# Kernel optimization log

Hardware: AMD Instinct MI355X
Metric: run time of the kernel (lower is better)

The kernel has to match this reference:

```python
import jax, jax.numpy as jnp
import numpy as np

B, N_L, N_T, C_IN, HID, NG, ATOMS, N_EDGES = 8, 128, 512, 128, 128, 10, 24, 4096
BN_EPS = 1e-5


def setup_inputs() -> dict:
    key = jax.random.key(0)
    ks = jax.random.split(key, 20)
    f32 = jnp.float32
    s = 0.05  # weight scale
    return {
        "h_l_x": jax.random.normal(ks[0], (B, N_L, C_IN), f32),
        "h_t_x": jax.random.normal(ks[1], (B, N_T, C_IN), f32),
        "l_mask": jnp.ones((B, N_L), dtype=bool),
        "t_mask": jnp.ones((B, N_T), dtype=bool),
        "h_l_pos": jax.random.normal(ks[2], (B, N_L, 3), f32),
        "h_t_pos": jax.random.normal(ks[3], (B, N_T * ATOMS, 3), f32),
        "x_l_flat": jax.random.normal(ks[4], (B * N_L, C_IN), f32),
        "edge_index": jax.random.randint(ks[5], (2, N_EDGES), 0, B * N_L),
        "W1": jax.random.normal(ks[6], (2 * C_IN, HID), f32) * s,
        "b1": jnp.zeros((HID,), f32),
        "bn_gamma": jnp.ones((HID,), f32),
        "bn_beta": jnp.zeros((HID,), f32),
        "bn_mean": jnp.zeros((HID,), f32),
        "bn_var": jnp.ones((HID,), f32),
        "W_pi": jax.random.normal(ks[7], (HID, NG), f32) * s,
        "b_pi": jnp.zeros((NG,), f32),
        "W_sigma": jax.random.normal(ks[8], (HID, NG), f32) * s,
        "b_sigma": jnp.zeros((NG,), f32),
        "W_mu": jax.random.normal(ks[9], (HID, NG), f32) * s,
        "b_mu": jnp.zeros((NG,), f32),
        "W_nuc": jax.random.normal(ks[10], (C_IN, 12), f32) * s,
        "b_nuc": jnp.zeros((12,), f32),
        "W_bond": jax.random.normal(ks[11], (2 * C_IN, 4), f32) * s,
        "b_bond": jnp.zeros((4,), f32),
    }


def reference(h_l_x, h_t_x, l_mask, t_mask, h_l_pos, h_t_pos, x_l_flat, edge_index,
              W1, b1, bn_gamma, bn_beta, bn_mean, bn_var,
              W_pi, b_pi, W_sigma, b_sigma, W_mu, b_mu,
              W_nuc, b_nuc, W_bond, b_bond):
    Bsz, Nl, Cd = h_l_x.shape
    Nt = h_t_x.shape[1]
    # dense pairwise concat: [B, N_l, N_t, 2C] (masks are all-True, so the
    # boolean selection C[C_mask] of the original is a static flatten)
    pair = jnp.concatenate([
        jnp.broadcast_to(h_l_x[:, :, None, :], (Bsz, Nl, Nt, Cd)),
        jnp.broadcast_to(h_t_x[:, None, :, :], (Bsz, Nl, Nt, Cd)),
    ], axis=-1).reshape(-1, 2 * Cd)
    # MLP: Linear -> BatchNorm1d (eval, running stats) -> ELU -> Dropout(eval=id)
    h = pair @ W1 + b1
    h = (h - bn_mean) * jax.lax.rsqrt(bn_var + BN_EPS) * bn_gamma + bn_beta
    h = jax.nn.elu(h)
    # MDN heads
    pi = jax.nn.softmax(h @ W_pi + b_pi, axis=-1)
    sigma = jax.nn.elu(h @ W_sigma + b_sigma) + 1.1
    mu = jax.nn.elu(h @ W_mu + b_mu) + 1.0
    # auxiliary heads on flat ligand node features
    nuc_types = x_l_flat @ W_nuc + b_nuc
    bond_feat = jnp.concatenate([x_l_flat[edge_index[0]], x_l_flat[edge_index[1]]], axis=1)
    bond_types = bond_feat @ W_bond + b_bond
    # pairwise distances with windowed min over 24 atoms per target residue
    d2 = (-2.0 * jnp.einsum('bld,btd->blt', h_l_pos, h_t_pos)
          + jnp.sum(h_t_pos ** 2, axis=-1)[:, None, :]
          + jnp.sum(h_l_pos ** 2, axis=-1)[:, :, None])
    d = jnp.nan_to_num(jnp.sqrt(d2), nan=10000.0)  # nan from sqrt(<0)
    dist = d.reshape(Bsz, Nl, Nt, ATOMS).min(axis=-1)  # [B, N_l, N_t]
    dist = jax.lax.stop_gradient(dist.reshape(-1)[:, None])  # detached, [M,1]
    C_batch = jnp.broadcast_to(jnp.arange(Bsz)[:, None, None], (Bsz, Nl, Nt)).reshape(-1)
    return (pi, sigma, mu, dist, nuc_types, bond_types, C_batch)
```

## Files before the change

### kernel.cpp

```cpp
#include <hip/hip_runtime.h>

#define B_      8
#define N_L     128
#define N_T     512
#define C_IN    128
#define HID     128
#define NG      10
#define ATOMS   24
#define N_EDGES 4096

#define OFF_PI  0
#define OFF_SG  5242880
#define OFF_MU  10485760
#define OFF_DI  15728640
#define OFF_NU  16252928
#define OFF_BO  16265216
#define OFF_CB  16281600

#define WS_U    0
#define WS_V    131072
#define WS_B    659456
#define WS_WT   659488

typedef unsigned short u16;
typedef unsigned int   u32;
typedef short s16x8 __attribute__((ext_vector_type(8)));
typedef float f32x4 __attribute__((ext_vector_type(4)));
typedef float f32x16 __attribute__((ext_vector_type(16)));
typedef u32   u32x4 __attribute__((ext_vector_type(4)));

__device__ __forceinline__ float bfu2f(u16 s) {
  u32 u = ((u32)s) << 16;
  return __builtin_bit_cast(float, u);
}
__device__ __forceinline__ u16 f2bf(float f) {
  u32 u = __builtin_bit_cast(u32, f);
  u32 r = (u + 0x7fffu + ((u >> 16) & 1u)) >> 16;
  return (u16)r;
}
__device__ __forceinline__ u32 pack2(float a, float b) {
  return (u32)f2bf(a) | ((u32)f2bf(b) << 16);
}
__device__ __forceinline__ u32 pkhi(float hi, float lo) {
  return __builtin_amdgcn_perm(__builtin_bit_cast(u32, hi),
                               __builtin_bit_cast(u32, lo), 0x07060302u);
}
__device__ __forceinline__ float eluf(float x) {
  return x > 0.f ? x : __expf(x) - 1.f;
}
__device__ __forceinline__ s16x8 ld8(const u16* p) {
  return __builtin_bit_cast(s16x8, *(const u32x4*)p);
}

template<bool F32>
__device__ __forceinline__ float ldf(const void* p, size_t i) {
  if constexpr (F32) return ((const float*)p)[i];
  else               return bfu2f(((const u16*)p)[i]);
}
template<bool F32>
__device__ __forceinline__ u16 wraw(const void* p, size_t i) {
  if constexpr (F32) return f2bf(((const float*)p)[i]);
  else               return ((const u16*)p)[i];
}
__device__ __forceinline__ bool is_f32(const u32* probe) {
  return (probe[0] & 0xFFFFu) == 0u;
}

template<bool F32>
__device__ __forceinline__ void prep_rows(
    int blk, int tid,
    const void* hlx, const void* htx, const void* W1, const void* b1,
    const void* gam, const void* bet, const void* mean_, const void* var_,
    float* __restrict__ ws, float (*xs)[C_IN]) {
  int k = tid & 127, g = tid >> 7;
  bool isU = (blk < 128);
  const void* x = isU ? hlx : htx;
  int row0 = isU ? blk * 8 : (blk - 128) * 8;
  size_t woff = isU ? 0 : (size_t)C_IN * HID;
  #pragma unroll
  for (int i = 0; i < 4; ++i) {
    int e = tid + i * 256;
    int rr = e >> 7, cc = e & 127;
    xs[rr][cc] = ldf<F32>(x, (size_t)(row0 + rr) * C_IN + cc);
  }
  __syncthreads();
  float a0 = 0.f, a1 = 0.f, a2 = 0.f, a3 = 0.f;
  const float* xr0 = xs[g * 4 + 0];
  const float* xr1 = xs[g * 4 + 1];
  const float* xr2 = xs[g * 4 + 2];
  const float* xr3 = xs[g * 4 + 3];
  #pragma unroll 8
  for (int c = 0; c < C_IN; ++c) {
    float w = ldf<F32>(W1, woff + (size_t)c * HID + k);
    a0 += xr0[c] * w;
    a1 += xr1[c] * w;
    a2 += xr2[c] * w;
    a3 += xr3[c] * w;
  }
  float A = ldf<F32>(gam, k) * rsqrtf(ldf<F32>(var_, k) + 1e-5f);
  float add = 0.f;
  if (isU) add = ldf<F32>(b1, k) * A + (ldf<F32>(bet, k) - ldf<F32>(mean_, k) * A);
  float* dst = ws + (isU ? WS_U : WS_V) + (size_t)row0 * HID;
  dst[(g * 4 + 0) * HID + k] = a0 * A + add;
  dst[(g * 4 + 1) * HID + k] = a1 * A + add;
  dst[(g * 4 + 2) * HID + k] = a2 * A + add;
  dst[(g * 4 + 3) * HID + k] = a3 * A + add;
}

template<bool F32>
__device__ __forceinline__ void prep_consts(
    int tid, const void* Wpi, const void* bpi, const void* Wsg, const void* bsg,
    const void* Wmu, const void* bmu, float* __restrict__ ws) {
  if (tid >= 128) return;
  int k = tid;
  u16* wt = (u16*)(ws + WS_WT);
  for (int j = 0; j < 32; ++j) {
    u16 val = 0;
    if (j < 10)      val = wraw<F32>(Wpi, (size_t)k * NG + j);
    else if (j < 20) val = wraw<F32>(Wsg, (size_t)k * NG + j - 10);
    else if (j < 30) val = wraw<F32>(Wmu, (size_t)k * NG + j - 20);
    wt[(size_t)j * HID + k] = val;
  }
  if (k < 32) {
    float bb = 0.f;
    if (k < 10)      bb = ldf<F32>(bpi, k);
    else if (k < 20) bb = ldf<F32>(bsg, k - 10);
    else if (k < 30) bb = ldf<F32>(bmu, k - 20);
    ws[WS_B + k] = bb;
  }
}

template<bool F32>
__device__ __forceinline__ void dist_impl(int blk2,
                                          const void* __restrict__ lpos,
                                          const void* __restrict__ tpos,
                                          void* __restrict__ out) {
  int lc   = blk2 & 63;
  int half = (blk2 >> 6) & 1;
  int b    = blk2 >> 7;
  int t = half * 256 + threadIdx.x;

  size_t tbase = ((size_t)b * (N_T * ATOMS) + (size_t)t * ATOMS) * 3;
  float ax[ATOMS], ay[ATOMS], az[ATOMS], an[ATOMS];
  if constexpr (F32) {
    float c[72];
    const float4* tp4 = (const float4*)((const float*)tpos + tbase);
    #pragma unroll
    for (int i = 0; i < 18; ++i) {
      float4 qv = tp4[i];
      c[4*i+0] = qv.x; c[4*i+1] = qv.y; c[4*i+2] = qv.z; c[4*i+3] = qv.w;
    }
    #pragma unroll
    for (int a = 0; a < ATOMS; ++a) {
      ax[a] = c[3*a]; ay[a] = c[3*a+1]; az[a] = c[3*a+2];
      an[a] = ax[a]*ax[a] + ay[a]*ay[a] + az[a]*az[a];
    }
  } else {
    u32 raw[36];
    const uint4* tp4 = (const uint4*)((const u16*)tpos + tbase);
    #pragma unroll
    for (int i = 0; i < 9; ++i) {
      uint4 qv = tp4[i];
      raw[4*i+0] = qv.x; raw[4*i+1] = qv.y; raw[4*i+2] = qv.z; raw[4*i+3] = qv.w;
    }
    #pragma unroll
    for (int a = 0; a < ATOMS; ++a) {
      int e = 3 * a;
      u32 w0 = raw[e >> 1];
      ax[a] = bfu2f((e & 1) ? (u16)(w0 >> 16) : (u16)w0);
      u32 w1 = raw[(e + 1) >> 1];
      ay[a] = bfu2f(((e + 1) & 1) ? (u16)(w1 >> 16) : (u16)w1);
      u32 w2 = raw[(e + 2) >> 1];
      az[a] = bfu2f(((e + 2) & 1) ? (u16)(w2 >> 16) : (u16)w2);
      an[a] = ax[a]*ax[a] + ay[a]*ay[a] + az[a]*az[a];
    }
  }
  #pragma unroll
  for (int il = 0; il < 2; ++il) {
    int l = lc * 2 + il;
    size_t lbase = ((size_t)b * N_L + l) * 3;
    float lx = ldf<F32>(lpos, lbase), ly = ldf<F32>(lpos, lbase+1), lz = ldf<F32>(lpos, lbase+2);
    float ln = lx*lx + ly*ly + lz*lz;
    float m = 1e30f;
    #pragma unroll
    for (int a = 0; a < ATOMS; ++a) {
      float dot = ax[a]*lx + ay[a]*ly + az[a]*lz;
      float d2 = ln + an[a] - 2.f * dot;
      d2 = (d2 >= 0.f) ? d2 : 1e30f;
      m = fminf(m, d2);
    }
    float d = (m < 1e29f) ? sqrtf(m) : 10000.0f;
    long p = ((long)(b * N_L + l)) * N_T + t;
    if constexpr (F32) {
      ((float*)out)[OFF_DI + p] = d;
      ((float*)out)[OFF_CB + p] = (float)b;
    } else {
      ((u16*)out)[OFF_DI + p] = f2bf(d);
      ((u16*)out)[OFF_CB + p] = f2bf((float)b);
    }
  }
}

__global__ __launch_bounds__(256) void prep_fused(
    const void* hlx, const void* htx, const void* W1, const void* b1,
    const void* gam, const void* bet, const void* mean_, const void* var_,
    const void* Wpi, const void* bpi, const void* Wsg, const void* bsg,
    const void* Wmu, const void* bmu, float* ws,
    const void* lpos, const void* tpos, void* out, const u32* probe) {
  __shared__ float xs[8][C_IN];
  int blk = blockIdx.x;
  int tid = threadIdx.x;
  bool f = is_f32(probe);
  if (blk < 640) {
    if (f) prep_rows<true >(blk, tid, hlx, htx, W1, b1, gam, bet, mean_, var_, ws, xs);
    else   prep_rows<false>(blk, tid, hlx, htx, W1, b1, gam, bet, mean_, var_, ws, xs);
  } else if (blk == 640) {
    if (f) prep_consts<true >(tid, Wpi, bpi, Wsg, bsg, Wmu, bmu, ws);
    else   prep_consts<false>(tid, Wpi, bpi, Wsg, bsg, Wmu, bmu, ws);
  } else {
    int blk2 = blk - 641;
    if (f) dist_impl<true >(blk2, lpos, tpos, out);
    else   dist_impl<false>(blk2, lpos, tpos, out);
  }
}

template<bool F32>
__device__ __forceinline__ void nuc_wave(int r, int lane, const void* __restrict__ xl,
    const void* __restrict__ Wnu, const void* __restrict__ bnu, void* __restrict__ out) {
  float x0 = ldf<F32>(xl, (size_t)r * C_IN + lane);
  float x1 = ldf<F32>(xl, (size_t)r * C_IN + 64 + lane);
  #pragma unroll
  for (int j = 0; j < 12; ++j) {
    float a = x0 * ldf<F32>(Wnu, (size_t)lane * 12 + j)
            + x1 * ldf<F32>(Wnu, (size_t)(64 + lane) * 12 + j);
    #pragma unroll
    for (int m = 32; m >= 1; m >>= 1) a += __shfl_xor(a, m);
    if (lane == 0) {
      float v = a + ldf<F32>(bnu, j);
      if constexpr (F32) ((float*)out)[OFF_NU + (size_t)r * 12 + j] = v;
      else               ((u16*)out)[OFF_NU + (size_t)r * 12 + j] = f2bf(v);
    }
  }
}

template<bool F32>
__device__ __forceinline__ void bond_wave(int e, int lane, const void* __restrict__ xl,
    const int* __restrict__ eidx, const void* __restrict__ Wbo,
    const void* __restrict__ bbo, void* __restrict__ out) {
  int e0 = eidx[e], e1 = eidx[N_EDGES + e];
  float x0 = ldf<F32>(xl, (size_t)e0 * C_IN + lane);
  float x1 = ldf<F32>(xl, (size_t)e0 * C_IN + 64 + lane);
  float y0 = ldf<F32>(xl, (size_t)e1 * C_IN + lane);
  float y1 = ldf<F32>(xl, (size_t)e1 * C_IN + 64 + lane);
  #pragma unroll
  for (int j = 0; j < 4; ++j) {
    float a = x0 * ldf<F32>(Wbo, (size_t)lane * 4 + j)
            + x1 * ldf<F32>(Wbo, (size_t)(64 + lane) * 4 + j)
            + y0 * ldf<F32>(Wbo, (size_t)(128 + lane) * 4 + j)
            + y1 * ldf<F32>(Wbo, (size_t)(192 + lane) * 4 + j);
    #pragma unroll
    for (int m = 32; m >= 1; m >>= 1) a += __shfl_xor(a, m);
    if (lane == 0) {
      float v = a + ldf<F32>(bbo, j);
      if constexpr (F32) ((float*)out)[OFF_BO + (size_t)e * 4 + j] = v;
      else               ((u16*)out)[OFF_BO + (size_t)e * 4 + j] = f2bf(v);
    }
  }
}

__global__ __launch_bounds__(256, 4) void main_fused(
    const float* __restrict__ ws, void* __restrict__ out, const u32* probe,
    const void* __restrict__ xl, const int* __restrict__ eidx,
    const void* __restrict__ Wnu, const void* __restrict__ bnu,
    const void* __restrict__ Wbo, const void* __restrict__ bbo) {
  __shared__ __align__(16) float stage[3840];
  __shared__ float u_lds[C_IN];
  int blk = blockIdx.x;
  int tid = threadIdx.x;
  int lane = tid & 63, wave = tid >> 6;
  bool f32o = is_f32(probe);

  if (blk >= 1024) {
    if (blk < 1024 + 256) {
      int r = (blk - 1024) * 4 + wave;
      if (f32o) nuc_wave<true >(r, lane, xl, Wnu, bnu, out);
      else      nuc_wave<false>(r, lane, xl, Wnu, bnu, out);
    } else {
      int e = (blk - 1280) * 4 + wave;
      if (f32o) bond_wave<true >(e, lane, xl, eidx, Wbo, bbo, out);
      else      bond_wave<false>(e, lane, xl, eidx, Wbo, bbo, out);
    }
    return;
  }

  int bl = blk;
  int b  = bl >> 7;
  int j  = lane & 31;
  int hi = lane >> 5;

  if (tid < C_IN) u_lds[tid] = ws[WS_U + (size_t)bl * HID + tid];
  __syncthreads();

  const u16* wt = (const u16*)(ws + WS_WT);
  s16x8 wf[8];
  #pragma unroll
  for (int ks = 0; ks < 8; ++ks)
    wf[ks] = ld8(wt + (size_t)j * HID + ks * 16 + hi * 8);

  float binit[16];
  #pragma unroll
  for (int r = 0; r < 16; ++r)
    binit[r] = ws[WS_B + ((r & 3) + 8 * (r >> 2) + 4 * hi)];

  const float* vbase = ws + WS_V + (size_t)b * N_T * HID;

  #pragma unroll 1
  for (int it = 0; it < 4; ++it) {
    int t = it * 128 + wave * 32 + j;
    const float* vp = vbase + (size_t)t * HID;

    f32x16 acc;
    #pragma unroll
    for (int r = 0; r < 16; ++r) acc[r] = binit[r];

    #pragma unroll
    for (int ks = 0; ks < 8; ++ks) {
      int ko = ks * 16 + hi * 8;
      f32x4 va = *(const f32x4*)(vp + ko);
      f32x4 vb = *(const f32x4*)(vp + ko + 4);
      f32x4 ua = *(const f32x4*)(u_lds + ko);
      f32x4 ub = *(const f32x4*)(u_lds + ko + 4);
      float h0 = eluf(va[0] + ua[0]);
      float h1 = eluf(va[1] + ua[1]);
      float h2 = eluf(va[2] + ua[2]);
      float h3 = eluf(va[3] + ua[3]);
      float h4 = eluf(vb[0] + ub[0]);
      float h5 = eluf(vb[1] + ub[1]);
      float h6 = eluf(vb[2] + ub[2]);
      float h7 = eluf(vb[3] + ub[3]);
      u32x4 hw = { pkhi(h1,h0), pkhi(h3,h2), pkhi(h5,h4), pkhi(h7,h6) };
      s16x8 hf = __builtin_bit_cast(s16x8, hw);
      acc = __builtin_amdgcn_mfma_f32_32x32x16_bf16(wf[ks], hf, acc, 0, 0, 0);
    }

    float pm = fmaxf(fmaxf(acc[0], acc[1]), fmaxf(acc[2], acc[3]));
    if (hi == 0) pm = fmaxf(pm, fmaxf(acc[4], acc[5]));
    pm = fmaxf(pm, __shfl_xor(pm, 32));
    float e0 = __expf(acc[0] - pm), e1 = __expf(acc[1] - pm);
    float e2 = __expf(acc[2] - pm), e3 = __expf(acc[3] - pm);
    float e4 = 0.f, e5 = 0.f;
    float es = e0 + e1 + e2 + e3;
    if (hi == 0) {
      e4 = __expf(acc[4] - pm); e5 = __expf(acc[5] - pm);
      es += e4 + e5;
    }
    es += __shfl_xor(es, 32);
    float inv = 1.f / es;

    int tl = wave * 32 + j;
    float* r0 = stage +        tl * 10;
    float* r1 = stage + 1280 + tl * 10;
    float* r2 = stage + 2560 + tl * 10;
    if (hi == 0) {
      r0[0] = e0*inv; r0[1] = e1*inv; r0[2] = e2*inv; r0[3] = e3*inv;
      r0[8] = e4*inv; r0[9] = e5*inv;
      r1[0] = eluf(acc[6])+1.1f;  r1[1] = eluf(acc[7])+1.1f;
      r1[6] = eluf(acc[8])+1.1f;  r1[7] = eluf(acc[9])+1.1f;
      r1[8] = eluf(acc[10])+1.1f; r1[9] = eluf(acc[11])+1.1f;
      r2[4] = eluf(acc[12])+1.0f; r2[5] = eluf(acc[13])+1.0f;
      r2[6] = eluf(acc[14])+1.0f; r2[7] = eluf(acc[15])+1.0f;
    } else {
      r0[4] = e0*inv; r0[5] = e1*inv; r0[6] = e2*inv; r0[7] = e3*inv;
      r1[2] = eluf(acc[4])+1.1f;  r1[3] = eluf(acc[5])+1.1f;
      r1[4] = eluf(acc[6])+1.1f;  r1[5] = eluf(acc[7])+1.1f;
      r2[0] = eluf(acc[8])+1.0f;  r2[1] = eluf(acc[9])+1.0f;
      r2[2] = eluf(acc[10])+1.0f; r2[3] = eluf(acc[11])+1.0f;
      r2[8] = eluf(acc[12])+1.0f; r2[9] = eluf(acc[13])+1.0f;
    }
    __syncthreads();

    size_t rowbase = ((size_t)bl * N_T + (size_t)it * 128) * NG;
    if (f32o) {
      float* o = (float*)out;
      #pragma unroll
      for (int g0 = 0; g0 < 4; ++g0) {
        int g = g0 * 256 + tid;
        if (g < 960) {
          int region = g / 320;
          int off = (g - region * 320) * 4;
          f32x4 v = *(const f32x4*)(stage + region * 1280 + off);
          size_t ob = (region == 0 ? (size_t)OFF_PI
                      : region == 1 ? (size_t)OFF_SG : (size_t)OFF_MU)
                      + rowbase + off;
          *(f32x4*)(o + ob) = v;
        }
      }
    } else {
      u16* o = (u16*)out;
      #pragma unroll
      for (int g0 = 0; g0 < 2; ++g0) {
        int g = g0 * 256 + tid;
        if (g < 480) {
          int region = g / 160;
          int off = (g - region * 160) * 8;
          const float* s = stage + region * 1280 + off;
          u32x4 v = { pack2(s[0],s[1]), pack2(s[2],s[3]),
                      pack2(s[4],s[5]), pack2(s[6],s[7]) };
          size_t ob = (region == 0 ? (size_t)OFF_PI
                      : region == 1 ? (size_t)OFF_SG : (size_t)OFF_MU)
                      + rowbase + off;
          *(u32x4*)(o + ob) = v;
        }
      }
    }
    __syncthreads();
  }
}

extern "C" void kernel_launch(void* const* d_in, const int* in_sizes, int n_in,
                              void* d_out, int out_size, void* d_ws, size_t ws_size,
                              hipStream_t stream) {
  int s = (n_in >= 24) ? 2 : 0;
  const void* hlx  = d_in[0];
  const void* htx  = d_in[1];
  const void* lpos = d_in[2 + s];
  const void* tpos = d_in[3 + s];
  const void* xl   = d_in[4 + s];
  const int*  eidx = (const int*)d_in[5 + s];
  const void* W1   = d_in[6 + s];
  const void* b1   = d_in[7 + s];
  const void* gam  = d_in[8 + s];
  const void* bet  = d_in[9 + s];
  const void* mean_= d_in[10 + s];
  const void* var_ = d_in[11 + s];
  const void* Wpi  = d_in[12 + s];
  const void* bpi  = d_in[13 + s];
  const void* Wsg  = d_in[14 + s];
  const void* bsg  = d_in[15 + s];
  const void* Wmu  = d_in[16 + s];
  const void* bmu  = d_in[17 + s];
  const void* Wnu  = d_in[18 + s];
  const void* bnu  = d_in[19 + s];
  const void* Wbo  = d_in[20 + s];
  const void* bbo  = d_in[21 + s];
  const u32* probe = (const u32*)var_;
  float* ws = (float*)d_ws;

  prep_fused<<<1665, 256, 0, stream>>>(hlx, htx, W1, b1, gam, bet, mean_, var_,
                                       Wpi, bpi, Wsg, bsg, Wmu, bmu, ws,
                                       lpos, tpos, d_out, probe);
  main_fused<<<2304, 256, 0, stream>>>(ws, d_out, probe,
                                       xl, eidx, Wnu, bnu, Wbo, bbo);
}
```

Before: 175.7 us.

## Move distance blocks into main kernel and use per-wave output staging

```diff
diff --git a/kernel.cpp b/kernel.cpp
--- a/kernel.cpp
+++ b/kernel.cpp
@@ -130,83 +130,11 @@
   }
 }
 
-template<bool F32>
-__device__ __forceinline__ void dist_impl(int blk2,
-                                          const void* __restrict__ lpos,
-                                          const void* __restrict__ tpos,
-                                          void* __restrict__ out) {
-  int lc   = blk2 & 63;
-  int half = (blk2 >> 6) & 1;
-  int b    = blk2 >> 7;
-  int t = half * 256 + threadIdx.x;
-
-  size_t tbase = ((size_t)b * (N_T * ATOMS) + (size_t)t * ATOMS) * 3;
-  float ax[ATOMS], ay[ATOMS], az[ATOMS], an[ATOMS];
-  if constexpr (F32) {
-    float c[72];
-    const float4* tp4 = (const float4*)((const float*)tpos + tbase);
-    #pragma unroll
-    for (int i = 0; i < 18; ++i) {
-      float4 qv = tp4[i];
-      c[4*i+0] = qv.x; c[4*i+1] = qv.y; c[4*i+2] = qv.z; c[4*i+3] = qv.w;
-    }
-    #pragma unroll
-    for (int a = 0; a < ATOMS; ++a) {
-      ax[a] = c[3*a]; ay[a] = c[3*a+1]; az[a] = c[3*a+2];
-      an[a] = ax[a]*ax[a] + ay[a]*ay[a] + az[a]*az[a];
-    }
-  } else {
-    u32 raw[36];
-    const uint4* tp4 = (const uint4*)((const u16*)tpos + tbase);
-    #pragma unroll
-    for (int i = 0; i < 9; ++i) {
-      uint4 qv = tp4[i];
-      raw[4*i+0] = qv.x; raw[4*i+1] = qv.y; raw[4*i+2] = qv.z; raw[4*i+3] = qv.w;
-    }
-    #pragma unroll
-    for (int a = 0; a < ATOMS; ++a) {
-      int e = 3 * a;
-      u32 w0 = raw[e >> 1];
-      ax[a] = bfu2f((e & 1) ? (u16)(w0 >> 16) : (u16)w0);
-      u32 w1 = raw[(e + 1) >> 1];
-      ay[a] = bfu2f(((e + 1) & 1) ? (u16)(w1 >> 16) : (u16)w1);
-      u32 w2 = raw[(e + 2) >> 1];
-      az[a] = bfu2f(((e + 2) & 1) ? (u16)(w2 >> 16) : (u16)w2);
-      an[a] = ax[a]*ax[a] + ay[a]*ay[a] + az[a]*az[a];
-    }
-  }
-  #pragma unroll
-  for (int il = 0; il < 2; ++il) {
-    int l = lc * 2 + il;
-    size_t lbase = ((size_t)b * N_L + l) * 3;
-    float lx = ldf<F32>(lpos, lbase), ly = ldf<F32>(lpos, lbase+1), lz = ldf<F32>(lpos, lbase+2);
-    float ln = lx*lx + ly*ly + lz*lz;
-    float m = 1e30f;
-    #pragma unroll
-    for (int a = 0; a < ATOMS; ++a) {
-      float dot = ax[a]*lx + ay[a]*ly + az[a]*lz;
-      float d2 = ln + an[a] - 2.f * dot;
-      d2 = (d2 >= 0.f) ? d2 : 1e30f;
-      m = fminf(m, d2);
-    }
-    float d = (m < 1e29f) ? sqrtf(m) : 10000.0f;
-    long p = ((long)(b * N_L + l)) * N_T + t;
-    if constexpr (F32) {
-      ((float*)out)[OFF_DI + p] = d;
-      ((float*)out)[OFF_CB + p] = (float)b;
-    } else {
-      ((u16*)out)[OFF_DI + p] = f2bf(d);
-      ((u16*)out)[OFF_CB + p] = f2bf((float)b);
-    }
-  }
-}
-
 __global__ __launch_bounds__(256) void prep_fused(
     const void* hlx, const void* htx, const void* W1, const void* b1,
     const void* gam, const void* bet, const void* mean_, const void* var_,
     const void* Wpi, const void* bpi, const void* Wsg, const void* bsg,
-    const void* Wmu, const void* bmu, float* ws,
-    const void* lpos, const void* tpos, void* out, const u32* probe) {
+    const void* Wmu, const void* bmu, float* ws, const u32* probe) {
   __shared__ float xs[8][C_IN];
   int blk = blockIdx.x;
   int tid = threadIdx.x;
@@ -214,13 +142,94 @@
   if (blk < 640) {
     if (f) prep_rows<true >(blk, tid, hlx, htx, W1, b1, gam, bet, mean_, var_, ws, xs);
     else   prep_rows<false>(blk, tid, hlx, htx, W1, b1, gam, bet, mean_, var_, ws, xs);
-  } else if (blk == 640) {
+  } else {
     if (f) prep_consts<true >(tid, Wpi, bpi, Wsg, bsg, Wmu, bmu, ws);
     else   prep_consts<false>(tid, Wpi, bpi, Wsg, bsg, Wmu, bmu, ws);
+  }
+}
+
+template<bool F32>
+__device__ __forceinline__ void dist_stream(int blk2, int tid,
+                                            const void* __restrict__ lpos,
+                                            const void* __restrict__ tpos,
+                                            void* __restrict__ out) {
+  int lc   = blk2 & 63;
+  int half = (blk2 >> 6) & 1;
+  int b    = blk2 >> 7;
+  int t = half * 256 + tid;
+
+  int l0 = lc * 2;
+  size_t lb0 = ((size_t)b * N_L + l0) * 3;
+  float lx0 = ldf<F32>(lpos, lb0+0), ly0 = ldf<F32>(lpos, lb0+1), lz0 = ldf<F32>(lpos, lb0+2);
+  float lx1 = ldf<F32>(lpos, lb0+3), ly1 = ldf<F32>(lpos, lb0+4), lz1 = ldf<F32>(lpos, lb0+5);
+  float ln0 = lx0*lx0 + ly0*ly0 + lz0*lz0;
+  float ln1 = lx1*lx1 + ly1*ly1 + lz1*lz1;
+  float m0 = 1e30f, m1 = 1e30f;
+
+  size_t tbase = ((size_t)b * (N_T * ATOMS) + (size_t)t * ATOMS) * 3;
+  if constexpr (F32) {
+    const float4* tp4 = (const float4*)((const float*)tpos + tbase);
+    #pragma unroll 1
+    for (int c4 = 0; c4 < 6; ++c4) {
+      float4 q0 = tp4[3*c4+0], q1 = tp4[3*c4+1], q2 = tp4[3*c4+2];
+      float ax[4] = {q0.x, q0.w, q1.z, q2.y};
+      float ay[4] = {q0.y, q1.x, q1.w, q2.z};
+      float az[4] = {q0.z, q1.y, q2.x, q2.w};
+      #pragma unroll
+      for (int a = 0; a < 4; ++a) {
+        float an = ax[a]*ax[a] + ay[a]*ay[a] + az[a]*az[a];
+        float d0 = ax[a]*lx0 + ay[a]*ly0 + az[a]*lz0;
+        float d1 = ax[a]*lx1 + ay[a]*ly1 + az[a]*lz1;
+        float e0 = ln0 + an - 2.f * d0;
+        float e1 = ln1 + an - 2.f * d1;
+        e0 = (e0 >= 0.f) ? e0 : 1e30f;
+        e1 = (e1 >= 0.f) ? e1 : 1e30f;
+        m0 = fminf(m0, e0);
+        m1 = fminf(m1, e1);
+      }
+    }
   } else {
-    int blk2 = blk - 641;
-    if (f) dist_impl<true >(blk2, lpos, tpos, out);
-    else   dist_impl<false>(blk2, lpos, tpos, out);
+    const uint4* tp4 = (const uint4*)((const u16*)tpos + tbase);
+    #pragma unroll 1
+    for (int c8 = 0; c8 < 3; ++c8) {
+      uint4 q0 = tp4[3*c8+0], q1 = tp4[3*c8+1], q2 = tp4[3*c8+2];
+      u32 w[12] = {q0.x,q0.y,q0.z,q0.w, q1.x,q1.y,q1.z,q1.w, q2.x,q2.y,q2.z,q2.w};
+      #pragma unroll
+      for (int a = 0; a < 8; ++a) {
+        int e = 3 * a;
+        u32 w0 = w[e >> 1];
+        float ax = bfu2f((e & 1) ? (u16)(w0 >> 16) : (u16)w0);
+        u32 w1 = w[(e + 1) >> 1];
+        float ay = bfu2f(((e + 1) & 1) ? (u16)(w1 >> 16) : (u16)w1);
+        u32 w2 = w[(e + 2) >> 1];
+        float az = bfu2f(((e + 2) & 1) ? (u16)(w2 >> 16) : (u16)w2);
+        float an = ax*ax + ay*ay + az*az;
+        float d0 = ax*lx0 + ay*ly0 + az*lz0;
+        float d1 = ax*lx1 + ay*ly1 + az*lz1;
+        float e0 = ln0 + an - 2.f * d0;
+        float e1 = ln1 + an - 2.f * d1;
+        e0 = (e0 >= 0.f) ? e0 : 1e30f;
+        e1 = (e1 >= 0.f) ? e1 : 1e30f;
+        m0 = fminf(m0, e0);
+        m1 = fminf(m1, e1);
+      }
+    }
+  }
+
+  float d0 = (m0 < 1e29f) ? sqrtf(m0) : 10000.0f;
+  float d1 = (m1 < 1e29f) ? sqrtf(m1) : 10000.0f;
+  long p0 = ((long)(b * N_L + l0)) * N_T + t;
+  long p1 = p0 + N_T;
+  if constexpr (F32) {
+    ((float*)out)[OFF_DI + p0] = d0;
+    ((float*)out)[OFF_DI + p1] = d1;
+    ((float*)out)[OFF_CB + p0] = (float)b;
+    ((float*)out)[OFF_CB + p1] = (float)b;
+  } else {
+    ((u16*)out)[OFF_DI + p0] = f2bf(d0);
+    ((u16*)out)[OFF_DI + p1] = f2bf(d1);
+    ((u16*)out)[OFF_CB + p0] = f2bf((float)b);
+    ((u16*)out)[OFF_CB + p1] = f2bf((float)b);
   }
 }
 
@@ -272,8 +281,9 @@
     const float* __restrict__ ws, void* __restrict__ out, const u32* probe,
     const void* __restrict__ xl, const int* __restrict__ eidx,
     const void* __restrict__ Wnu, const void* __restrict__ bnu,
-    const void* __restrict__ Wbo, const void* __restrict__ bbo) {
-  __shared__ __align__(16) float stage[3840];
+    const void* __restrict__ Wbo, const void* __restrict__ bbo,
+    const void* __restrict__ lpos, const void* __restrict__ tpos) {
+  __shared__ __align__(16) float stage[4][960];
   __shared__ float u_lds[C_IN];
   int blk = blockIdx.x;
   int tid = threadIdx.x;
@@ -281,12 +291,16 @@
   bool f32o = is_f32(probe);
 
   if (blk >= 1024) {
-    if (blk < 1024 + 256) {
-      int r = (blk - 1024) * 4 + wave;
+    if (blk < 2048) {
+      int blk2 = blk - 1024;
+      if (f32o) dist_stream<true >(blk2, tid, lpos, tpos, out);
+      else      dist_stream<false>(blk2, tid, lpos, tpos, out);
+    } else if (blk < 2048 + 256) {
+      int r = (blk - 2048) * 4 + wave;
       if (f32o) nuc_wave<true >(r, lane, xl, Wnu, bnu, out);
       else      nuc_wave<false>(r, lane, xl, Wnu, bnu, out);
     } else {
-      int e = (blk - 1280) * 4 + wave;
+      int e = (blk - 2304) * 4 + wave;
       if (f32o) bond_wave<true >(e, lane, xl, eidx, Wbo, bbo, out);
       else      bond_wave<false>(e, lane, xl, eidx, Wbo, bbo, out);
     }
@@ -313,6 +327,7 @@
     binit[r] = ws[WS_B + ((r & 3) + 8 * (r >> 2) + 4 * hi)];
 
   const float* vbase = ws + WS_V + (size_t)b * N_T * HID;
+  float* sw = stage[wave];
 
   #pragma unroll 1
   for (int it = 0; it < 4; ++it) {
@@ -357,10 +372,9 @@
     es += __shfl_xor(es, 32);
     float inv = 1.f / es;
 
-    int tl = wave * 32 + j;
-    float* r0 = stage +        tl * 10;
-    float* r1 = stage + 1280 + tl * 10;
-    float* r2 = stage + 2560 + tl * 10;
+    float* r0 = sw +       j * 10;
+    float* r1 = sw + 320 + j * 10;
+    float* r2 = sw + 640 + j * 10;
     if (hi == 0) {
       r0[0] = e0*inv; r0[1] = e1*inv; r0[2] = e2*inv; r0[3] = e3*inv;
       r0[8] = e4*inv; r0[9] = e5*inv;
@@ -377,43 +391,37 @@
       r2[2] = eluf(acc[10])+1.0f; r2[3] = eluf(acc[11])+1.0f;
       r2[8] = eluf(acc[12])+1.0f; r2[9] = eluf(acc[13])+1.0f;
     }
-    __syncthreads();
-
-    size_t rowbase = ((size_t)bl * N_T + (size_t)it * 128) * NG;
+
+    size_t rowbase = ((size_t)bl * N_T + (size_t)it * 128 + (size_t)wave * 32) * NG;
     if (f32o) {
       float* o = (float*)out;
       #pragma unroll
-      for (int g0 = 0; g0 < 4; ++g0) {
-        int g = g0 * 256 + tid;
-        if (g < 960) {
-          int region = g / 320;
-          int off = (g - region * 320) * 4;
-          f32x4 v = *(const f32x4*)(stage + region * 1280 + off);
-          size_t ob = (region == 0 ? (size_t)OFF_PI
-                      : region == 1 ? (size_t)OFF_SG : (size_t)OFF_MU)
-                      + rowbase + off;
-          *(f32x4*)(o + ob) = v;
+      for (int rg = 0; rg < 3; ++rg) {
+        size_t ob = (rg == 0 ? (size_t)OFF_PI : rg == 1 ? (size_t)OFF_SG : (size_t)OFF_MU)
+                    + rowbase;
+        #pragma unroll
+        for (int g = 0; g < 2; ++g) {
+          int idx = g * 64 + lane;
+          if (idx < 80) {
+            f32x4 v = *(const f32x4*)(sw + rg * 320 + idx * 4);
+            *(f32x4*)(o + ob + idx * 4) = v;
+          }
         }
       }
     } else {
       u16* o = (u16*)out;
       #pragma unroll
-      for (int g0 = 0; g0 < 2; ++g0) {
-        int g = g0 * 256 + tid;
-        if (g < 480) {
-          int region = g / 160;
-          int off = (g - region * 160) * 8;
-          const float* s = stage + region * 1280 + off;
+      for (int rg = 0; rg < 3; ++rg) {
+        size_t ob = (rg == 0 ? (size_t)OFF_PI : rg == 1 ? (size_t)OFF_SG : (size_t)OFF_MU)
+                    + rowbase;
+        if (lane < 40) {
+          const float* s = sw + rg * 320 + lane * 8;
           u32x4 v = { pack2(s[0],s[1]), pack2(s[2],s[3]),
                       pack2(s[4],s[5]), pack2(s[6],s[7]) };
-          size_t ob = (region == 0 ? (size_t)OFF_PI
-                      : region == 1 ? (size_t)OFF_SG : (size_t)OFF_MU)
-                      + rowbase + off;
-          *(u32x4*)(o + ob) = v;
+          *(u32x4*)(o + ob + lane * 8) = v;
         }
       }
     }
-    __syncthreads();
   }
 }
 
@@ -446,9 +454,8 @@
   const u32* probe = (const u32*)var_;
   float* ws = (float*)d_ws;
 
-  prep_fused<<<1665, 256, 0, stream>>>(hlx, htx, W1, b1, gam, bet, mean_, var_,
-                                       Wpi, bpi, Wsg, bsg, Wmu, bmu, ws,
-                                       lpos, tpos, d_out, probe);
-  main_fused<<<2304, 256, 0, stream>>>(ws, d_out, probe,
-                                       xl, eidx, Wnu, bnu, Wbo, bbo);
-}
+  prep_fused<<<641, 256, 0, stream>>>(hlx, htx, W1, b1, gam, bet, mean_, var_,
+                                      Wpi, bpi, Wsg, bsg, Wmu, bmu, ws, probe);
+  main_fused<<<3328, 256, 0, stream>>>(ws, d_out, probe,
+                                       xl, eidx, Wnu, bnu, Wbo, bbo, lpos, tpos);
+}
```

Result: slower. 194.8 us (+10.9%).

## Use per-wave output staging and split each ligand row across two blocks

Applied to the files above, without the earlier changes.

```diff
diff --git a/kernel.cpp b/kernel.cpp
--- a/kernel.cpp
+++ b/kernel.cpp
@@ -273,30 +273,31 @@
     const void* __restrict__ xl, const int* __restrict__ eidx,
     const void* __restrict__ Wnu, const void* __restrict__ bnu,
     const void* __restrict__ Wbo, const void* __restrict__ bbo) {
-  __shared__ __align__(16) float stage[3840];
+  __shared__ __align__(16) float stage[4][960];
   __shared__ float u_lds[C_IN];
   int blk = blockIdx.x;
   int tid = threadIdx.x;
   int lane = tid & 63, wave = tid >> 6;
   bool f32o = is_f32(probe);
 
-  if (blk >= 1024) {
-    if (blk < 1024 + 256) {
-      int r = (blk - 1024) * 4 + wave;
+  if (blk >= 2048) {
+    if (blk < 2048 + 256) {
+      int r = (blk - 2048) * 4 + wave;
       if (f32o) nuc_wave<true >(r, lane, xl, Wnu, bnu, out);
       else      nuc_wave<false>(r, lane, xl, Wnu, bnu, out);
     } else {
-      int e = (blk - 1280) * 4 + wave;
+      int e = (blk - 2304) * 4 + wave;
       if (f32o) bond_wave<true >(e, lane, xl, eidx, Wbo, bbo, out);
       else      bond_wave<false>(e, lane, xl, eidx, Wbo, bbo, out);
     }
     return;
   }
 
-  int bl = blk;
-  int b  = bl >> 7;
-  int j  = lane & 31;
-  int hi = lane >> 5;
+  int bl  = blk >> 1;
+  int ith = blk & 1;
+  int b   = bl >> 7;
+  int j   = lane & 31;
+  int hi  = lane >> 5;
 
   if (tid < C_IN) u_lds[tid] = ws[WS_U + (size_t)bl * HID + tid];
   __syncthreads();
@@ -313,9 +314,11 @@
     binit[r] = ws[WS_B + ((r & 3) + 8 * (r >> 2) + 4 * hi)];
 
   const float* vbase = ws + WS_V + (size_t)b * N_T * HID;
+  float* sw = stage[wave];
 
   #pragma unroll 1
-  for (int it = 0; it < 4; ++it) {
+  for (int i2 = 0; i2 < 2; ++i2) {
+    int it = ith * 2 + i2;
     int t = it * 128 + wave * 32 + j;
     const float* vp = vbase + (size_t)t * HID;
 
@@ -357,10 +360,9 @@
     es += __shfl_xor(es, 32);
     float inv = 1.f / es;
 
-    int tl = wave * 32 + j;
-    float* r0 = stage +        tl * 10;
-    float* r1 = stage + 1280 + tl * 10;
-    float* r2 = stage + 2560 + tl * 10;
+    float* r0 = sw +       j * 10;
+    float* r1 = sw + 320 + j * 10;
+    float* r2 = sw + 640 + j * 10;
     if (hi == 0) {
       r0[0] = e0*inv; r0[1] = e1*inv; r0[2] = e2*inv; r0[3] = e3*inv;
       r0[8] = e4*inv; r0[9] = e5*inv;
@@ -377,43 +379,37 @@
       r2[2] = eluf(acc[10])+1.0f; r2[3] = eluf(acc[11])+1.0f;
       r2[8] = eluf(acc[12])+1.0f; r2[9] = eluf(acc[13])+1.0f;
     }
-    __syncthreads();
-
-    size_t rowbase = ((size_t)bl * N_T + (size_t)it * 128) * NG;
+
+    size_t rowbase = ((size_t)bl * N_T + (size_t)it * 128 + (size_t)wave * 32) * NG;
     if (f32o) {
       float* o = (float*)out;
       #pragma unroll
-      for (int g0 = 0; g0 < 4; ++g0) {
-        int g = g0 * 256 + tid;
-        if (g < 960) {
-          int region = g / 320;
-          int off = (g - region * 320) * 4;
-          f32x4 v = *(const f32x4*)(stage + region * 1280 + off);
-          size_t ob = (region == 0 ? (size_t)OFF_PI
-                      : region == 1 ? (size_t)OFF_SG : (size_t)OFF_MU)
-                      + rowbase + off;
-          *(f32x4*)(o + ob) = v;
+      for (int rg = 0; rg < 3; ++rg) {
+        size_t ob = (rg == 0 ? (size_t)OFF_PI : rg == 1 ? (size_t)OFF_SG : (size_t)OFF_MU)
+                    + rowbase;
+        #pragma unroll
+        for (int g = 0; g < 2; ++g) {
+          int idx = g * 64 + lane;
+          if (idx < 80) {
+            f32x4 v = *(const f32x4*)(sw + rg * 320 + idx * 4);
+            *(f32x4*)(o + ob + idx * 4) = v;
+          }
         }
       }
     } else {
       u16* o = (u16*)out;
       #pragma unroll
-      for (int g0 = 0; g0 < 2; ++g0) {
-        int g = g0 * 256 + tid;
-        if (g < 480) {
-          int region = g / 160;
-          int off = (g - region * 160) * 8;
-          const float* s = stage + region * 1280 + off;
+      for (int rg = 0; rg < 3; ++rg) {
+        size_t ob = (rg == 0 ? (size_t)OFF_PI : rg == 1 ? (size_t)OFF_SG : (size_t)OFF_MU)
+                    + rowbase;
+        if (lane < 40) {
+          const float* s = sw + rg * 320 + lane * 8;
           u32x4 v = { pack2(s[0],s[1]), pack2(s[2],s[3]),
                       pack2(s[4],s[5]), pack2(s[6],s[7]) };
-          size_t ob = (region == 0 ? (size_t)OFF_PI
-                      : region == 1 ? (size_t)OFF_SG : (size_t)OFF_MU)
-                      + rowbase + off;
-          *(u32x4*)(o + ob) = v;
+          *(u32x4*)(o + ob + lane * 8) = v;
         }
       }
     }
-    __syncthreads();
   }
 }
 
@@ -449,6 +445,6 @@
   prep_fused<<<1665, 256, 0, stream>>>(hlx, htx, W1, b1, gam, bet, mean_, var_,
                                        Wpi, bpi, Wsg, bsg, Wmu, bmu, ws,
                                        lpos, tpos, d_out, probe);
-  main_fused<<<2304, 256, 0, stream>>>(ws, d_out, probe,
+  main_fused<<<3328, 256, 0, stream>>>(ws, d_out, probe,
                                        xl, eidx, Wnu, bnu, Wbo, bbo);
 }
```

Result: slower. 203.7 us (+15.9%).
